# Kernel tuning notes

Measured on AMD Instinct MI355X. Metric: run time of the kernel, lower is better.

The kernel has to match this reference:

```python
import jax, jax.numpy as jnp
import numpy as np

N, E, D, H = 40000, 640000, 128, 8
DH = D // H  # out_feats per head
EPS = 1e-5


def _layernorm(x, g, b):
    mu = jnp.mean(x, axis=-1, keepdims=True)
    var = jnp.mean(jnp.square(x - mu), axis=-1, keepdims=True)
    return (x - mu) * jax.lax.rsqrt(var + EPS) * g + b


def setup_inputs() -> dict:
    key = jax.random.key(0)
    ks = jax.random.split(key, 12)
    s = 0.02
    return {
        "feat": jax.random.normal(ks[0], (N, D), dtype=jnp.float32),
        "src": jax.random.randint(ks[1], (E,), 0, N, dtype=jnp.int32),
        "dst": jax.random.randint(ks[2], (E,), 0, N, dtype=jnp.int32),
        "Wq": jax.random.normal(ks[3], (D, D), dtype=jnp.float32) * s,
        "Wk": jax.random.normal(ks[4], (D, D), dtype=jnp.float32) * s,
        "Wv": jax.random.normal(ks[5], (D, D), dtype=jnp.float32) * s,
        "ln1_g": jnp.ones((D,), jnp.float32),
        "ln1_b": jnp.zeros((D,), jnp.float32),
        "ln2_g": jnp.ones((D,), jnp.float32),
        "ln2_b": jnp.zeros((D,), jnp.float32),
        "W1": jax.random.normal(ks[6], (D, 4 * D), dtype=jnp.float32) * s,
        "b1": jnp.zeros((4 * D,), jnp.float32),
        "prelu_w": jnp.full((4 * D,), 0.25, jnp.float32),
        "W2": jax.random.normal(ks[7], (4 * D, D), dtype=jnp.float32) * s,
        "b2": jnp.zeros((D,), jnp.float32),
    }


def reference(feat, src, dst, Wq, Wk, Wv, ln1_g, ln1_b, ln2_g, ln2_b,
              W1, b1, prelu_w, W2, b2):
    n = feat.shape[0]
    feat_c = jax.lax.stop_gradient(feat)  # .clone().detach()
    q = (feat @ Wq).reshape(n, H, DH)
    k = (feat_c @ Wk).reshape(n, H, DH)
    v = (feat_c @ Wv).reshape(n, H, DH)

    # u_dot_v: per-edge, per-head dot product of k at src and q at dst
    scores = jnp.einsum('ehd,ehd->eh', k[src], q[dst]) / np.float32(np.sqrt(DH * H))

    # edge_softmax: softmax over incoming edges of each destination node
    smax = jax.ops.segment_max(scores, dst, num_segments=n)  # [N,H]
    sexp = jnp.exp(scores - smax[dst])
    ssum = jax.ops.segment_sum(sexp, dst, num_segments=n)
    a = sexp / ssum[dst]  # [E,H]  (attn_drop is eval no-op)

    # u_mul_e + sum: weighted scatter-aggregate of v[src] into dst
    msgs = v[src] * a[:, :, None]  # [E,H,DH]
    ft2 = jax.ops.segment_sum(msgs, dst, num_segments=n).reshape(n, D)

    rst = _layernorm(ft2 + feat, ln1_g, ln1_b)
    h = rst @ W1 + b1
    h = jnp.where(h >= 0, h, prelu_w * h)  # PReLU, per-channel
    ffn = h @ W2 + b2  # ffn_drop is eval no-op
    return _layernorm(rst + ffn, ln2_g, ln2_b)
```

## Files before the change

### kernel.cpp

```cpp
#include <hip/hip_runtime.h>
#include <hip/hip_bf16.h>
#include <math.h>

#define DIM 128
#define NHEAD 8
#define DHEAD 16
#define HID 512
#define LN_EPS 1e-5f
#define QSCALE 0.12751879104863297f

typedef __bf16 bf16x8 __attribute__((ext_vector_type(8)));
typedef float f32x4 __attribute__((ext_vector_type(4)));
typedef _Float16 f16x2 __attribute__((ext_vector_type(2)));

__device__ inline float bf2f(unsigned int bits16) {
    return __uint_as_float(bits16 << 16);
}
__device__ inline unsigned short f2bf(float f) {
    unsigned int u = __float_as_uint(f);
    unsigned int r = u + 0x7fff + ((u >> 16) & 1);
    return (unsigned short)(r >> 16);
}
__device__ inline unsigned short f2h(float f) {
    _Float16 h = (_Float16)f;
    return __builtin_bit_cast(unsigned short, h);
}
__device__ inline float edot2(unsigned int kw, f16x2 q) {
#if __has_builtin(__builtin_amdgcn_fdot2)
    return __builtin_amdgcn_fdot2(__builtin_bit_cast(f16x2, kw), q, 0.f, false);
#else
    f16x2 k = __builtin_bit_cast(f16x2, kw);
    return (float)k.x * (float)q.x + (float)k.y * (float)q.y;
#endif
}
__device__ inline float fexp2(float x) {
#if __has_builtin(__builtin_amdgcn_exp2f)
    return __builtin_amdgcn_exp2f(x);
#else
    return exp2f(x);
#endif
}

__device__ inline void gload_lds16(const void* g, void* l) {
    __builtin_amdgcn_global_load_lds(
        (const __attribute__((address_space(1))) unsigned int*)g,
        (__attribute__((address_space(3))) unsigned int*)l, 16, 0, 0);
}

__global__ __launch_bounds__(256) void prep_kernel(
        int* counts, int Nn,
        const float* __restrict__ feat, unsigned short* __restrict__ featb,
        const float* __restrict__ Wq, const float* __restrict__ Wk, const float* __restrict__ Wv,
        unsigned short* __restrict__ Wqkvt,
        const float* __restrict__ W1, unsigned short* __restrict__ W1t,
        const float* __restrict__ W2, unsigned short* __restrict__ W2t,
        int zb, int fb) {
    int blk = blockIdx.x, t = threadIdx.x;
    if (blk < zb) {
        int i = blk * 1024 + t * 4;
        if (i < Nn) *(int4*)(counts + i) = make_int4(0, 0, 0, 0);
    } else if (blk < fb) {
        int i = (blk - zb) * 256 + t;
        if (i < Nn * 32) {
            float4 v = *(const float4*)(feat + (size_t)i * 4);
            ushort4 o;
            o.x = f2bf(v.x); o.y = f2bf(v.y); o.z = f2bf(v.z); o.w = f2bf(v.w);
            *(ushort4*)(featb + (size_t)i * 4) = o;
        }
    } else {
        int b2_ = blk - fb;
        if (b2_ < 192) {
            int sec = b2_ >> 6;
            const float* W = sec == 0 ? Wq : (sec == 1 ? Wk : Wv);
            int o = (b2_ & 63) * 256 + t;
            int oc = o >> 7, orow = o & 127;
            Wqkvt[sec * 16384 + o] = f2bf(W[(size_t)orow * 128 + oc]);
        } else if (b2_ < 448) {
            int o = (b2_ - 192) * 256 + t;
            int oc = o >> 7, orow = o & 127;
            W1t[o] = f2bf(W1[(size_t)orow * 512 + oc]);
        } else {
            int o = (b2_ - 448) * 256 + t;
            int oc = o >> 9, orow = o & 511;
            W2t[o] = f2bf(W2[(size_t)orow * 128 + oc]);
        }
    }
}


__global__ void count_kernel(const int* __restrict__ dst, int* counts, int E) {
    int e = blockIdx.x * blockDim.x + threadIdx.x;
    if (e < E) atomicAdd(&counts[dst[e]], 1);
}

__global__ __launch_bounds__(256) void scanA_kernel(const int* __restrict__ counts, int* bsum, int Nn) {
    int blk = blockIdx.x, t = threadIdx.x;
    int i = blk * 1024 + t * 4;
    int s = 0;
    if (i < Nn) { int4 x = *(const int4*)(counts + i); s = x.x + x.y + x.z + x.w; }
#pragma unroll
    for (int off = 1; off < 64; off <<= 1) s += __shfl_xor(s, off, 64);
    __shared__ int wt[4];
    if ((t & 63) == 0) wt[t >> 6] = s;
    __syncthreads();
    if (t == 0) bsum[blk] = wt[0] + wt[1] + wt[2] + wt[3];
}

__global__ __launch_bounds__(256) void scanC_kernel(int* counts, const int* __restrict__ bsum,
                                                    int* offsets, int Nn, int NCH) {
    int blk = blockIdx.x, t = threadIdx.x, lane = t & 63, wv = t >> 6;
    __shared__ int wt[4];
    __shared__ int base_s;
    if (wv == 0) {
        int v = (lane < NCH) ? bsum[lane] : 0;
        int s = v;
#pragma unroll
        for (int off = 1; off < 64; off <<= 1) {
            int u = __shfl_up(s, off, 64);
            if (lane >= off) s += u;
        }
        int basev = (blk > 0) ? __shfl(s, blk - 1, 64) : 0;
        int tot = __shfl(s, NCH - 1, 64);
        if (lane == 0) {
            base_s = basev;
            if (blk == 0) offsets[Nn] = tot;
        }
    }
    int i = blk * 1024 + t * 4;
    int4 x = make_int4(0, 0, 0, 0);
    if (i < Nn) x = *(const int4*)(counts + i);
    int ts = x.x + x.y + x.z + x.w;
    int s = ts;
#pragma unroll
    for (int off = 1; off < 64; off <<= 1) {
        int u = __shfl_up(s, off, 64);
        if (lane >= off) s += u;
    }
    if (lane == 63) wt[wv] = s;
    __syncthreads();
    int woff = 0;
    for (int wi = 0; wi < wv; ++wi) woff += wt[wi];
    int excl = base_s + woff + (s - ts);
    if (i < Nn) {
        int o0 = excl, o1 = o0 + x.x, o2 = o1 + x.y, o3 = o2 + x.z;
        *(int4*)(offsets + i) = make_int4(o0, o1, o2, o3);
        *(int4*)(counts + i) = make_int4(o0, o1, o2, o3);
    }
}

__global__ void fill_kernel(const int* __restrict__ dst, const int* __restrict__ src,
                            int* cursor, int* srcs, int E) {
    int e = blockIdx.x * blockDim.x + threadIdx.x;
    if (e < E) {
        int pos = atomicAdd(&cursor[dst[e]], 1);
        srcs[pos] = src[e];
    }
}

#define QST 136
__global__ __launch_bounds__(256) void qkv_gemm(
        const unsigned short* __restrict__ A, const unsigned short* __restrict__ Bt,
        unsigned short* __restrict__ qb, unsigned short* __restrict__ kb,
        unsigned short* __restrict__ vb) {
    __shared__ unsigned short smem[128 * QST];
    unsigned short* As = smem;
    unsigned short* Bs = smem + 4096;
    int t = threadIdx.x;
    int wave = t >> 6, lane = t & 63;
    int wr = wave >> 1, wc = wave & 1;
    int lrow = lane & 15, kq = lane >> 4;
    int m0 = blockIdx.y * 128;
    int region = blockIdx.x;
    int n0 = region * 128;
    int srow = t >> 2, scol8 = (t & 3) * 8;

    f32x4 acc[4][4] = {};
    for (int k0 = 0; k0 < 128; k0 += 32) {
        gload_lds16(A + (size_t)(m0 + srow) * 128 + k0 + scol8,      As + t * 8);
        gload_lds16(A + (size_t)(m0 + 64 + srow) * 128 + k0 + scol8, As + 2048 + t * 8);
        gload_lds16(Bt + (size_t)(n0 + srow) * 128 + k0 + scol8,      Bs + t * 8);
        gload_lds16(Bt + (size_t)(n0 + 64 + srow) * 128 + k0 + scol8, Bs + 2048 + t * 8);
        __syncthreads();
        bf16x8 af[4], bfr[4];
#pragma unroll
        for (int mi = 0; mi < 4; ++mi)
            af[mi] = *(const bf16x8*)(&As[(wr * 64 + mi * 16 + lrow) * 32 + kq * 8]);
#pragma unroll
        for (int ni = 0; ni < 4; ++ni)
            bfr[ni] = *(const bf16x8*)(&Bs[(wc * 64 + ni * 16 + lrow) * 32 + kq * 8]);
#pragma unroll
        for (int mi = 0; mi < 4; ++mi)
#pragma unroll
            for (int ni = 0; ni < 4; ++ni)
                acc[mi][ni] = __builtin_amdgcn_mfma_f32_16x16x32_bf16(af[mi], bfr[ni], acc[mi][ni], 0, 0, 0);
        __syncthreads();
    }

    float scale = (region == 0) ? QSCALE : 1.f;
#pragma unroll
    for (int ni = 0; ni < 4; ++ni) {
        int col = wc * 64 + ni * 16 + lrow;
#pragma unroll
        for (int mi = 0; mi < 4; ++mi) {
#pragma unroll
            for (int r = 0; r < 4; ++r) {
                int row = wr * 64 + mi * 16 + kq * 4 + r;
                smem[row * QST + col] = f2h(acc[mi][ni][r] * scale);
            }
        }
    }
    __syncthreads();
    unsigned short* outp = (region == 0 ? qb : (region == 1 ? kb : vb)) + (size_t)m0 * 128;
#pragma unroll
    for (int i = 0; i < 8; ++i) {
        int chunk = i * 256 + t;
        int row = chunk >> 4, c16 = chunk & 15;
        *(float4*)(outp + (size_t)chunk * 8) = *(const float4*)(smem + row * QST + c16 * 8);
    }
}

__global__ __launch_bounds__(256) void agg_ln1_kernel(
        const unsigned short* __restrict__ qb, const unsigned short* __restrict__ kb,
        const unsigned short* __restrict__ vb,
        const float* __restrict__ feat,
        const int* __restrict__ srcs, const int* __restrict__ offsets,
        const float* __restrict__ g, const float* __restrict__ b,
        unsigned short* __restrict__ rstb, int n) {
    int node = blockIdx.x * 4 + (threadIdx.x >> 6);
    int lane = threadIdx.x & 63;
    if (node >= n) return;

    const unsigned int* q32 = (const unsigned int*)qb;
    const unsigned int* k32 = (const unsigned int*)kb;
    const unsigned int* v32 = (const unsigned int*)vb;
    f16x2 qp = __builtin_bit_cast(f16x2, q32[(size_t)node * 64 + lane]);

    int beg = offsets[node], end = offsets[node + 1];
    float m = -INFINITY, l = 0.f, a0 = 0.f, a1 = 0.f;

    int idx = beg;
    for (; idx + 8 <= end; idx += 8) {
        int s[8];
#pragma unroll
        for (int i = 0; i < 8; ++i) s[i] = srcs[idx + i];
        unsigned int kw[8], vw[8];
#pragma unroll
        for (int i = 0; i < 8; ++i) kw[i] = k32[(size_t)s[i] * 64 + lane];
#pragma unroll
        for (int i = 0; i < 8; ++i) vw[i] = v32[(size_t)s[i] * 64 + lane];
        float sc[8];
#pragma unroll
        for (int i = 0; i < 8; ++i) {
            float p = edot2(kw[i], qp);
            p += __shfl_xor(p, 1, 8);
            p += __shfl_xor(p, 2, 8);
            p += __shfl_xor(p, 4, 8);
            sc[i] = p;
        }
        float mn = m;
#pragma unroll
        for (int i = 0; i < 8; ++i) mn = fmaxf(mn, sc[i]);
        float f = fexp2(m - mn);
        float wsum = 0.f, d0 = 0.f, d1 = 0.f;
#pragma unroll
        for (int i = 0; i < 8; ++i) {
            float w = fexp2(sc[i] - mn);
            f16x2 vp = __builtin_bit_cast(f16x2, vw[i]);
            wsum += w;
            d0 = fmaf((float)vp.x, w, d0);
            d1 = fmaf((float)vp.y, w, d1);
        }
        l = l * f + wsum;
        a0 = a0 * f + d0;
        a1 = a1 * f + d1;
        m = mn;
    }
    for (; idx < end; ++idx) {
        int s = srcs[idx];
        unsigned int kw = k32[(size_t)s * 64 + lane];
        unsigned int vw = v32[(size_t)s * 64 + lane];
        float p = edot2(kw, qp);
        p += __shfl_xor(p, 1, 8);
        p += __shfl_xor(p, 2, 8);
        p += __shfl_xor(p, 4, 8);
        float mn = fmaxf(m, p);
        float f = fexp2(m - mn), w = fexp2(p - mn);
        f16x2 vp = __builtin_bit_cast(f16x2, vw);
        l = l * f + w;
        a0 = a0 * f + w * (float)vp.x;
        a1 = a1 * f + w * (float)vp.y;
        m = mn;
    }

    float inv = (l > 0.f) ? 1.f / l : 0.f;
    float2 fv = *(const float2*)(feat + (size_t)node * DIM + 2 * lane);
    float x0 = a0 * inv + fv.x;
    float x1 = a1 * inv + fv.y;

    float s1 = x0 + x1;
    float s2 = x0 * x0 + x1 * x1;
#pragma unroll
    for (int off = 1; off < 64; off <<= 1) {
        s1 += __shfl_xor(s1, off, 64);
        s2 += __shfl_xor(s2, off, 64);
    }
    float mean = s1 * (1.f / DIM);
    float var = s2 * (1.f / DIM) - mean * mean;
    float rinv = rsqrtf(var + LN_EPS);
    float g0 = g[2 * lane], g1 = g[2 * lane + 1];
    float b0 = b[2 * lane], b1 = b[2 * lane + 1];
    float o0 = (x0 - mean) * rinv * g0 + b0;
    float o1 = (x1 - mean) * rinv * g1 + b1;
    unsigned int packed = (unsigned int)f2bf(o0) | ((unsigned int)f2bf(o1) << 16);
    ((unsigned int*)rstb)[(size_t)node * 64 + lane] = packed;
}

#define FST 136
__global__ __launch_bounds__(256, 2) void ffn_fused_kernel(
        const unsigned short* __restrict__ rstb,
        const unsigned short* __restrict__ W1t, const float* __restrict__ b1,
        const float* __restrict__ prelu,
        const unsigned short* __restrict__ W2t, const float* __restrict__ b2,
        const float* __restrict__ g, const float* __restrict__ bb,
        float* __restrict__ out, int Nn) {
    __shared__ unsigned short As[128 * FST];
    __shared__ unsigned short Hs[128 * FST];
    __shared__ unsigned short Bs[128 * 32];
    __shared__ float red[128][4];

    int t = threadIdx.x, wave = t >> 6, lane = t & 63;
    int lrow = lane & 15, kq = lane >> 4;
    int wr = wave >> 1, wc = wave & 1;
    int m0 = blockIdx.x * 128;
    int srow = t >> 2, scol8 = (t & 3) * 8;

    {
        int row = t >> 1, half = t & 1;
        const float4* src = (const float4*)(rstb + (size_t)(m0 + row) * 128 + half * 64);
        float4* dst = (float4*)(As + row * FST + half * 64);
#pragma unroll
        for (int i = 0; i < 8; ++i) dst[i] = src[i];
    }
    f32x4 facc[4][4] = {};
    __syncthreads();

    for (int c = 0; c < 4; ++c) {
        f32x4 hacc[4][4] = {};
        for (int k0 = 0; k0 < 128; k0 += 32) {
            gload_lds16(W1t + (size_t)(c * 128 + srow) * 128 + k0 + scol8,      Bs + t * 8);
            gload_lds16(W1t + (size_t)(c * 128 + 64 + srow) * 128 + k0 + scol8, Bs + 2048 + t * 8);
            __syncthreads();
            bf16x8 hf[4], nf[4];
#pragma unroll
            for (int hi = 0; hi < 4; ++hi)
                hf[hi] = *(const bf16x8*)(&Bs[(wr * 64 + hi * 16 + lrow) * 32 + kq * 8]);
#pragma unroll
            for (int nj = 0; nj < 4; ++nj)
                nf[nj] = *(const bf16x8*)(&As[(wc * 64 + nj * 16 + lrow) * FST + k0 + kq * 8]);
#pragma unroll
            for (int hi = 0; hi < 4; ++hi)
#pragma unroll
                for (int nj = 0; nj < 4; ++nj)
                    hacc[hi][nj] = __builtin_amdgcn_mfma_f32_16x16x32_bf16(hf[hi], nf[nj], hacc[hi][nj], 0, 0, 0);
            __syncthreads();
        }
#pragma unroll
        for (int hi = 0; hi < 4; ++hi) {
            int hloc = wr * 64 + hi * 16 + kq * 4;
#pragma unroll
            for (int r = 0; r < 4; ++r) {
                int hg = c * 128 + hloc + r;
                float biv = b1[hg], pwv = prelu[hg];
#pragma unroll
                for (int nj = 0; nj < 4; ++nj) {
                    int node = wc * 64 + nj * 16 + lrow;
                    float v = hacc[hi][nj][r] + biv;
                    v = v >= 0.f ? v : pwv * v;
                    Hs[node * FST + hloc + r] = f2bf(v);
                }
            }
        }
        __syncthreads();
        for (int k0 = 0; k0 < 128; k0 += 32) {
            gload_lds16(W2t + (size_t)srow * 512 + c * 128 + k0 + scol8,        Bs + t * 8);
            gload_lds16(W2t + (size_t)(64 + srow) * 512 + c * 128 + k0 + scol8, Bs + 2048 + t * 8);
            __syncthreads();
            bf16x8 af[4], bf2r[4];
#pragma unroll
            for (int mi = 0; mi < 4; ++mi)
                af[mi] = *(const bf16x8*)(&Hs[(wr * 64 + mi * 16 + lrow) * FST + k0 + kq * 8]);
#pragma unroll
            for (int ni = 0; ni < 4; ++ni)
                bf2r[ni] = *(const bf16x8*)(&Bs[(wc * 64 + ni * 16 + lrow) * 32 + kq * 8]);
#pragma unroll
            for (int mi = 0; mi < 4; ++mi)
#pragma unroll
                for (int ni = 0; ni < 4; ++ni)
                    facc[mi][ni] = __builtin_amdgcn_mfma_f32_16x16x32_bf16(af[mi], bf2r[ni], facc[mi][ni], 0, 0, 0);
            __syncthreads();
        }
    }

    float b2v[4], gv[4], bv[4];
    int cols[4];
#pragma unroll
    for (int ni = 0; ni < 4; ++ni) {
        cols[ni] = wc * 64 + ni * 16 + lrow;
        b2v[ni] = b2[cols[ni]]; gv[ni] = g[cols[ni]]; bv[ni] = bb[cols[ni]];
    }
#pragma unroll
    for (int mi = 0; mi < 4; ++mi) {
#pragma unroll
        for (int r = 0; r < 4; ++r) {
            int rloc = wr * 64 + mi * 16 + kq * 4 + r;
            int row = m0 + rloc;
            float ps = 0.f, pq = 0.f;
#pragma unroll
            for (int ni = 0; ni < 4; ++ni) {
                float rsv = bf2f(rstb[(size_t)row * 128 + cols[ni]]);
                float v = facc[mi][ni][r] + b2v[ni] + rsv;
                facc[mi][ni][r] = v;
                ps += v; pq += v * v;
            }
#pragma unroll
            for (int off = 1; off < 16; off <<= 1) {
                ps += __shfl_xor(ps, off, 16);
                pq += __shfl_xor(pq, off, 16);
            }
            if (lrow == 0) { red[rloc][wc * 2] = ps; red[rloc][wc * 2 + 1] = pq; }
        }
    }
    __syncthreads();
#pragma unroll
    for (int mi = 0; mi < 4; ++mi) {
#pragma unroll
        for (int r = 0; r < 4; ++r) {
            int rloc = wr * 64 + mi * 16 + kq * 4 + r;
            int row = m0 + rloc;
            float s1 = red[rloc][0] + red[rloc][2];
            float s2 = red[rloc][1] + red[rloc][3];
            float mean = s1 * (1.f / DIM);
            float var = s2 * (1.f / DIM) - mean * mean;
            float rs = rsqrtf(var + LN_EPS);
            if (row < Nn) {
#pragma unroll
                for (int ni = 0; ni < 4; ++ni)
                    out[(size_t)row * 128 + cols[ni]] =
                        (facc[mi][ni][r] - mean) * rs * gv[ni] + bv[ni];
            }
        }
    }
}


extern "C" void kernel_launch(void* const* d_in, const int* in_sizes, int n_in,
                              void* d_out, int out_size, void* d_ws, size_t ws_size,
                              hipStream_t stream) {
    const float* feat   = (const float*)d_in[0];
    const int*   src    = (const int*)d_in[1];
    const int*   dst    = (const int*)d_in[2];
    const float* Wq     = (const float*)d_in[3];
    const float* Wk     = (const float*)d_in[4];
    const float* Wv     = (const float*)d_in[5];
    const float* ln1_g  = (const float*)d_in[6];
    const float* ln1_b  = (const float*)d_in[7];
    const float* ln2_g  = (const float*)d_in[8];
    const float* ln2_b  = (const float*)d_in[9];
    const float* W1     = (const float*)d_in[10];
    const float* b1     = (const float*)d_in[11];
    const float* prelu  = (const float*)d_in[12];
    const float* W2     = (const float*)d_in[13];
    const float* b2     = (const float*)d_in[14];
    float* out = (float*)d_out;

    const int Nn = in_sizes[0] / DIM;
    const int E  = in_sizes[1];
    const int MP = (Nn + 127) & ~127;

    char* w = (char*)d_ws;
    unsigned short* qb   = (unsigned short*)w; w += (size_t)MP * DIM * 2;
    unsigned short* kb   = (unsigned short*)w; w += (size_t)MP * DIM * 2;
    unsigned short* vb   = (unsigned short*)w; w += (size_t)MP * DIM * 2;
    unsigned short* rstb = (unsigned short*)w; w += (size_t)MP * DIM * 2;
    unsigned short* featb= (unsigned short*)w; w += (size_t)MP * DIM * 2;
    unsigned short* Wqkvt= (unsigned short*)w; w += 3 * DIM * DIM * 2;
    unsigned short* W1t  = (unsigned short*)w; w += (size_t)HID * DIM * 2;
    unsigned short* W2t  = (unsigned short*)w; w += (size_t)DIM * HID * 2;
    int* counts  = (int*)w;  w += (size_t)Nn * 4;
    int* offsets = (int*)w;  w += (size_t)(Nn + 4) * 4;
    int* bsum    = (int*)w;  w += 64 * 4;
    int* srcs    = (int*)w;

    const int NCH = (Nn + 1023) / 1024;
    const int zb = NCH;
    const int fb = zb + Nn / 8;

    prep_kernel<<<fb + 192 + 256 + 256, 256, 0, stream>>>(
        counts, Nn, feat, featb, Wq, Wk, Wv, Wqkvt, W1, W1t, W2, W2t, zb, fb);

    count_kernel<<<(E + 255) / 256, 256, 0, stream>>>(dst, counts, E);
    scanA_kernel<<<NCH, 256, 0, stream>>>(counts, bsum, Nn);
    scanC_kernel<<<NCH, 256, 0, stream>>>(counts, bsum, offsets, Nn, NCH);
    fill_kernel<<<(E + 255) / 256, 256, 0, stream>>>(dst, src, counts, srcs, E);

    {
        dim3 grid(3, MP / 128);
        qkv_gemm<<<grid, 256, 0, stream>>>(featb, Wqkvt, qb, kb, vb);
    }

    agg_ln1_kernel<<<(Nn + 3) / 4, 256, 0, stream>>>(qb, kb, vb, feat, srcs, offsets,
                                                     ln1_g, ln1_b, rstb, Nn);

    ffn_fused_kernel<<<MP / 128, 256, 0, stream>>>(rstb, W1t, b1, prelu,
                                                   W2t, b2, ln2_g, ln2_b, out, Nn);
}
```

Before: 262.6 us.

## Pack K/V as interleaved FP8 and split fused FFN into two GEMM kernels

Result: slower. 280.6 us (+6.8%).

```diff
diff --git a/kernel.cpp b/kernel.cpp
--- a/kernel.cpp
+++ b/kernel.cpp
@@ -11,6 +11,7 @@
 
 typedef __bf16 bf16x8 __attribute__((ext_vector_type(8)));
 typedef float f32x4 __attribute__((ext_vector_type(4)));
+typedef float f32x2 __attribute__((ext_vector_type(2)));
 typedef _Float16 f16x2 __attribute__((ext_vector_type(2)));
 
 __device__ inline float bf2f(unsigned int bits16) {
@@ -25,21 +26,15 @@
     _Float16 h = (_Float16)f;
     return __builtin_bit_cast(unsigned short, h);
 }
-__device__ inline float edot2(unsigned int kw, f16x2 q) {
-#if __has_builtin(__builtin_amdgcn_fdot2)
-    return __builtin_amdgcn_fdot2(__builtin_bit_cast(f16x2, kw), q, 0.f, false);
-#else
-    f16x2 k = __builtin_bit_cast(f16x2, kw);
-    return (float)k.x * (float)q.x + (float)k.y * (float)q.y;
-#endif
-}
-__device__ inline float fexp2(float x) {
-#if __has_builtin(__builtin_amdgcn_exp2f)
-    return __builtin_amdgcn_exp2f(x);
-#else
-    return exp2f(x);
-#endif
-}
+__device__ inline unsigned short pk_fp8(float a, float b) {
+    int r = __builtin_amdgcn_cvt_pk_fp8_f32(a, b, 0, false);
+    return (unsigned short)(r & 0xffff);
+}
+template <bool HI>
+__device__ inline f32x2 unpk_fp8(unsigned int w) {
+    return __builtin_amdgcn_cvt_pk_f32_fp8((int)w, HI);
+}
+__device__ inline float fexp2(float x) { return __builtin_amdgcn_exp2f(x); }
 
 __device__ inline void gload_lds16(const void* g, void* l) {
     __builtin_amdgcn_global_load_lds(
@@ -160,8 +155,7 @@
 #define QST 136
 __global__ __launch_bounds__(256) void qkv_gemm(
         const unsigned short* __restrict__ A, const unsigned short* __restrict__ Bt,
-        unsigned short* __restrict__ qb, unsigned short* __restrict__ kb,
-        unsigned short* __restrict__ vb) {
+        unsigned short* __restrict__ qb, unsigned short* __restrict__ kvp) {
     __shared__ unsigned short smem[128 * QST];
     unsigned short* As = smem;
     unsigned short* Bs = smem + 4096;
@@ -210,18 +204,31 @@
         }
     }
     __syncthreads();
-    unsigned short* outp = (region == 0 ? qb : (region == 1 ? kb : vb)) + (size_t)m0 * 128;
-#pragma unroll
-    for (int i = 0; i < 8; ++i) {
-        int chunk = i * 256 + t;
-        int row = chunk >> 4, c16 = chunk & 15;
-        *(float4*)(outp + (size_t)chunk * 8) = *(const float4*)(smem + row * QST + c16 * 8);
+    if (region == 0) {
+        unsigned short* outp = qb + (size_t)m0 * 128;
+#pragma unroll
+        for (int i = 0; i < 8; ++i) {
+            int chunk = i * 256 + t;
+            int row = chunk >> 4, c16 = chunk & 15;
+            *(float4*)(outp + (size_t)chunk * 8) = *(const float4*)(smem + row * QST + c16 * 8);
+        }
+    } else {
+        int off = region - 1;
+        int row = t >> 1, half = t & 1;
+        unsigned short* dstp = kvp + (size_t)(m0 + row) * 128 + off;
+        const unsigned short* sp = smem + row * QST;
+#pragma unroll
+        for (int jj = 0; jj < 32; ++jj) {
+            int j = half * 32 + jj;
+            float f0 = (float)__builtin_bit_cast(_Float16, sp[2 * j]);
+            float f1 = (float)__builtin_bit_cast(_Float16, sp[2 * j + 1]);
+            dstp[2 * j] = pk_fp8(f0, f1);
+        }
     }
 }
 
 __global__ __launch_bounds__(256) void agg_ln1_kernel(
-        const unsigned short* __restrict__ qb, const unsigned short* __restrict__ kb,
-        const unsigned short* __restrict__ vb,
+        const unsigned short* __restrict__ qb, const unsigned short* __restrict__ kvp,
         const float* __restrict__ feat,
         const int* __restrict__ srcs, const int* __restrict__ offsets,
         const float* __restrict__ g, const float* __restrict__ b,
@@ -230,10 +237,10 @@
     int lane = threadIdx.x & 63;
     if (node >= n) return;
 
-    const unsigned int* q32 = (const unsigned int*)qb;
-    const unsigned int* k32 = (const unsigned int*)kb;
-    const unsigned int* v32 = (const unsigned int*)vb;
-    f16x2 qp = __builtin_bit_cast(f16x2, q32[(size_t)node * 64 + lane]);
+    unsigned int qw = ((const unsigned int*)qb)[(size_t)node * 64 + lane];
+    f16x2 qp = __builtin_bit_cast(f16x2, qw);
+    float q0 = (float)qp.x, q1 = (float)qp.y;
+    const unsigned int* kv32 = (const unsigned int*)kvp;
 
     int beg = offsets[node], end = offsets[node + 1];
     float m = -INFINITY, l = 0.f, a0 = 0.f, a1 = 0.f;
@@ -243,15 +250,14 @@
         int s[8];
 #pragma unroll
         for (int i = 0; i < 8; ++i) s[i] = srcs[idx + i];
-        unsigned int kw[8], vw[8];
-#pragma unroll
-        for (int i = 0; i < 8; ++i) kw[i] = k32[(size_t)s[i] * 64 + lane];
-#pragma unroll
-        for (int i = 0; i < 8; ++i) vw[i] = v32[(size_t)s[i] * 64 + lane];
+        unsigned int w[8];
+#pragma unroll
+        for (int i = 0; i < 8; ++i) w[i] = kv32[(size_t)s[i] * 64 + lane];
         float sc[8];
 #pragma unroll
         for (int i = 0; i < 8; ++i) {
-            float p = edot2(kw[i], qp);
+            f32x2 kk = unpk_fp8<false>(w[i]);
+            float p = fmaf(kk.x, q0, kk.y * q1);
             p += __shfl_xor(p, 1, 8);
             p += __shfl_xor(p, 2, 8);
             p += __shfl_xor(p, 4, 8);
@@ -264,11 +270,11 @@
         float wsum = 0.f, d0 = 0.f, d1 = 0.f;
 #pragma unroll
         for (int i = 0; i < 8; ++i) {
-            float w = fexp2(sc[i] - mn);
-            f16x2 vp = __builtin_bit_cast(f16x2, vw[i]);
-            wsum += w;
-            d0 = fmaf((float)vp.x, w, d0);
-            d1 = fmaf((float)vp.y, w, d1);
+            float ww = fexp2(sc[i] - mn);
+            f32x2 vv = unpk_fp8<true>(w[i]);
+            wsum += ww;
+            d0 = fmaf(vv.x, ww, d0);
+            d1 = fmaf(vv.y, ww, d1);
         }
         l = l * f + wsum;
         a0 = a0 * f + d0;
@@ -277,18 +283,18 @@
     }
     for (; idx < end; ++idx) {
         int s = srcs[idx];
-        unsigned int kw = k32[(size_t)s * 64 + lane];
-        unsigned int vw = v32[(size_t)s * 64 + lane];
-        float p = edot2(kw, qp);
+        unsigned int w = kv32[(size_t)s * 64 + lane];
+        f32x2 kk = unpk_fp8<false>(w);
+        float p = fmaf(kk.x, q0, kk.y * q1);
         p += __shfl_xor(p, 1, 8);
         p += __shfl_xor(p, 2, 8);
         p += __shfl_xor(p, 4, 8);
         float mn = fmaxf(m, p);
-        float f = fexp2(m - mn), w = fexp2(p - mn);
-        f16x2 vp = __builtin_bit_cast(f16x2, vw);
-        l = l * f + w;
-        a0 = a0 * f + w * (float)vp.x;
-        a1 = a1 * f + w * (float)vp.y;
+        float f = fexp2(m - mn), ww = fexp2(p - mn);
+        f32x2 vv = unpk_fp8<true>(w);
+        l = l * f + ww;
+        a0 = a0 * f + ww * vv.x;
+        a1 = a1 * f + ww * vv.y;
         m = mn;
     }
 
@@ -315,90 +321,104 @@
     ((unsigned int*)rstb)[(size_t)node * 64 + lane] = packed;
 }
 
-#define FST 136
-__global__ __launch_bounds__(256, 2) void ffn_fused_kernel(
+__global__ __launch_bounds__(256) void ffn1_gemm(
+        const unsigned short* __restrict__ A, const unsigned short* __restrict__ Bt,
+        unsigned short* __restrict__ hid,
+        const float* __restrict__ b1, const float* __restrict__ prelu) {
+    __shared__ unsigned short smem[128 * QST];
+    unsigned short* As = smem;
+    unsigned short* Bs = smem + 4096;
+    int t = threadIdx.x;
+    int wave = t >> 6, lane = t & 63;
+    int wr = wave >> 1, wc = wave & 1;
+    int lrow = lane & 15, kq = lane >> 4;
+    int m0 = blockIdx.y * 128;
+    int n0 = blockIdx.x * 128;
+    int srow = t >> 2, scol8 = (t & 3) * 8;
+
+    f32x4 acc[4][4] = {};
+    for (int k0 = 0; k0 < 128; k0 += 32) {
+        gload_lds16(A + (size_t)(m0 + srow) * 128 + k0 + scol8,      As + t * 8);
+        gload_lds16(A + (size_t)(m0 + 64 + srow) * 128 + k0 + scol8, As + 2048 + t * 8);
+        gload_lds16(Bt + (size_t)(n0 + srow) * 128 + k0 + scol8,      Bs + t * 8);
+        gload_lds16(Bt + (size_t)(n0 + 64 + srow) * 128 + k0 + scol8, Bs + 2048 + t * 8);
+        __syncthreads();
+        bf16x8 af[4], bfr[4];
+#pragma unroll
+        for (int mi = 0; mi < 4; ++mi)
+            af[mi] = *(const bf16x8*)(&As[(wr * 64 + mi * 16 + lrow) * 32 + kq * 8]);
+#pragma unroll
+        for (int ni = 0; ni < 4; ++ni)
+            bfr[ni] = *(const bf16x8*)(&Bs[(wc * 64 + ni * 16 + lrow) * 32 + kq * 8]);
+#pragma unroll
+        for (int mi = 0; mi < 4; ++mi)
+#pragma unroll
+            for (int ni = 0; ni < 4; ++ni)
+                acc[mi][ni] = __builtin_amdgcn_mfma_f32_16x16x32_bf16(af[mi], bfr[ni], acc[mi][ni], 0, 0, 0);
+        __syncthreads();
+    }
+
+#pragma unroll
+    for (int ni = 0; ni < 4; ++ni) {
+        int col = wc * 64 + ni * 16 + lrow;
+        int cg = n0 + col;
+        float biv = b1[cg], pwv = prelu[cg];
+#pragma unroll
+        for (int mi = 0; mi < 4; ++mi) {
+#pragma unroll
+            for (int r = 0; r < 4; ++r) {
+                int row = wr * 64 + mi * 16 + kq * 4 + r;
+                float v = acc[mi][ni][r] + biv;
+                v = v >= 0.f ? v : pwv * v;
+                smem[row * QST + col] = f2bf(v);
+            }
+        }
+    }
+    __syncthreads();
+#pragma unroll
+    for (int i = 0; i < 8; ++i) {
+        int chunk = i * 256 + t;
+        int row = chunk >> 4, c16 = chunk & 15;
+        *(float4*)(hid + (size_t)(m0 + row) * 512 + n0 + c16 * 8) =
+            *(const float4*)(smem + row * QST + c16 * 8);
+    }
+}
+
+__global__ __launch_bounds__(256) void ffn2_ln2_kernel(
+        const unsigned short* __restrict__ hid, const unsigned short* __restrict__ W2t,
         const unsigned short* __restrict__ rstb,
-        const unsigned short* __restrict__ W1t, const float* __restrict__ b1,
-        const float* __restrict__ prelu,
-        const unsigned short* __restrict__ W2t, const float* __restrict__ b2,
-        const float* __restrict__ g, const float* __restrict__ bb,
+        const float* __restrict__ b2, const float* __restrict__ g, const float* __restrict__ bb,
         float* __restrict__ out, int Nn) {
-    __shared__ unsigned short As[128 * FST];
-    __shared__ unsigned short Hs[128 * FST];
+    __shared__ unsigned short As[128 * 32];
     __shared__ unsigned short Bs[128 * 32];
     __shared__ float red[128][4];
-
-    int t = threadIdx.x, wave = t >> 6, lane = t & 63;
+    int t = threadIdx.x;
+    int wave = t >> 6, lane = t & 63;
+    int wr = wave >> 1, wc = wave & 1;
     int lrow = lane & 15, kq = lane >> 4;
-    int wr = wave >> 1, wc = wave & 1;
     int m0 = blockIdx.x * 128;
     int srow = t >> 2, scol8 = (t & 3) * 8;
 
-    {
-        int row = t >> 1, half = t & 1;
-        const float4* src = (const float4*)(rstb + (size_t)(m0 + row) * 128 + half * 64);
-        float4* dst = (float4*)(As + row * FST + half * 64);
-#pragma unroll
-        for (int i = 0; i < 8; ++i) dst[i] = src[i];
-    }
-    f32x4 facc[4][4] = {};
-    __syncthreads();
-
-    for (int c = 0; c < 4; ++c) {
-        f32x4 hacc[4][4] = {};
-        for (int k0 = 0; k0 < 128; k0 += 32) {
-            gload_lds16(W1t + (size_t)(c * 128 + srow) * 128 + k0 + scol8,      Bs + t * 8);
-            gload_lds16(W1t + (size_t)(c * 128 + 64 + srow) * 128 + k0 + scol8, Bs + 2048 + t * 8);
-            __syncthreads();
-            bf16x8 hf[4], nf[4];
-#pragma unroll
-            for (int hi = 0; hi < 4; ++hi)
-                hf[hi] = *(const bf16x8*)(&Bs[(wr * 64 + hi * 16 + lrow) * 32 + kq * 8]);
-#pragma unroll
-            for (int nj = 0; nj < 4; ++nj)
-                nf[nj] = *(const bf16x8*)(&As[(wc * 64 + nj * 16 + lrow) * FST + k0 + kq * 8]);
-#pragma unroll
-            for (int hi = 0; hi < 4; ++hi)
-#pragma unroll
-                for (int nj = 0; nj < 4; ++nj)
-                    hacc[hi][nj] = __builtin_amdgcn_mfma_f32_16x16x32_bf16(hf[hi], nf[nj], hacc[hi][nj], 0, 0, 0);
-            __syncthreads();
-        }
-#pragma unroll
-        for (int hi = 0; hi < 4; ++hi) {
-            int hloc = wr * 64 + hi * 16 + kq * 4;
-#pragma unroll
-            for (int r = 0; r < 4; ++r) {
-                int hg = c * 128 + hloc + r;
-                float biv = b1[hg], pwv = prelu[hg];
-#pragma unroll
-                for (int nj = 0; nj < 4; ++nj) {
-                    int node = wc * 64 + nj * 16 + lrow;
-                    float v = hacc[hi][nj][r] + biv;
-                    v = v >= 0.f ? v : pwv * v;
-                    Hs[node * FST + hloc + r] = f2bf(v);
-                }
-            }
-        }
+    f32x4 acc[4][4] = {};
+    for (int k0 = 0; k0 < 512; k0 += 32) {
+        gload_lds16(hid + (size_t)(m0 + srow) * 512 + k0 + scol8,      As + t * 8);
+        gload_lds16(hid + (size_t)(m0 + 64 + srow) * 512 + k0 + scol8, As + 2048 + t * 8);
+        gload_lds16(W2t + (size_t)srow * 512 + k0 + scol8,             Bs + t * 8);
+        gload_lds16(W2t + (size_t)(64 + srow) * 512 + k0 + scol8,      Bs + 2048 + t * 8);
         __syncthreads();
-        for (int k0 = 0; k0 < 128; k0 += 32) {
-            gload_lds16(W2t + (size_t)srow * 512 + c * 128 + k0 + scol8,        Bs + t * 8);
-            gload_lds16(W2t + (size_t)(64 + srow) * 512 + c * 128 + k0 + scol8, Bs + 2048 + t * 8);
-            __syncthreads();
-            bf16x8 af[4], bf2r[4];
-#pragma unroll
-            for (int mi = 0; mi < 4; ++mi)
-                af[mi] = *(const bf16x8*)(&Hs[(wr * 64 + mi * 16 + lrow) * FST + k0 + kq * 8]);
+        bf16x8 af[4], bfr[4];
+#pragma unroll
+        for (int mi = 0; mi < 4; ++mi)
+            af[mi] = *(const bf16x8*)(&As[(wr * 64 + mi * 16 + lrow) * 32 + kq * 8]);
+#pragma unroll
+        for (int ni = 0; ni < 4; ++ni)
+            bfr[ni] = *(const bf16x8*)(&Bs[(wc * 64 + ni * 16 + lrow) * 32 + kq * 8]);
+#pragma unroll
+        for (int mi = 0; mi < 4; ++mi)
 #pragma unroll
             for (int ni = 0; ni < 4; ++ni)
-                bf2r[ni] = *(const bf16x8*)(&Bs[(wc * 64 + ni * 16 + lrow) * 32 + kq * 8]);
-#pragma unroll
-            for (int mi = 0; mi < 4; ++mi)
-#pragma unroll
-                for (int ni = 0; ni < 4; ++ni)
-                    facc[mi][ni] = __builtin_amdgcn_mfma_f32_16x16x32_bf16(af[mi], bf2r[ni], facc[mi][ni], 0, 0, 0);
-            __syncthreads();
-        }
+                acc[mi][ni] = __builtin_amdgcn_mfma_f32_16x16x32_bf16(af[mi], bfr[ni], acc[mi][ni], 0, 0, 0);
+        __syncthreads();
     }
 
     float b2v[4], gv[4], bv[4];
@@ -418,8 +438,8 @@
 #pragma unroll
             for (int ni = 0; ni < 4; ++ni) {
                 float rsv = bf2f(rstb[(size_t)row * 128 + cols[ni]]);
-                float v = facc[mi][ni][r] + b2v[ni] + rsv;
-                facc[mi][ni][r] = v;
+                float v = acc[mi][ni][r] + b2v[ni] + rsv;
+                acc[mi][ni][r] = v;
                 ps += v; pq += v * v;
             }
 #pragma unroll
@@ -446,7 +466,7 @@
 #pragma unroll
                 for (int ni = 0; ni < 4; ++ni)
                     out[(size_t)row * 128 + cols[ni]] =
-                        (facc[mi][ni][r] - mean) * rs * gv[ni] + bv[ni];
+                        (acc[mi][ni][r] - mean) * rs * gv[ni] + bv[ni];
             }
         }
     }
@@ -479,10 +499,10 @@
 
     char* w = (char*)d_ws;
     unsigned short* qb   = (unsigned short*)w; w += (size_t)MP * DIM * 2;
-    unsigned short* kb   = (unsigned short*)w; w += (size_t)MP * DIM * 2;
-    unsigned short* vb   = (unsigned short*)w; w += (size_t)MP * DIM * 2;
+    unsigned short* kvp  = (unsigned short*)w; w += (size_t)MP * DIM * 2;
     unsigned short* rstb = (unsigned short*)w; w += (size_t)MP * DIM * 2;
     unsigned short* featb= (unsigned short*)w; w += (size_t)MP * DIM * 2;
+    unsigned short* hid  = (unsigned short*)w; w += (size_t)MP * HID * 2;
     unsigned short* Wqkvt= (unsigned short*)w; w += 3 * DIM * DIM * 2;
     unsigned short* W1t  = (unsigned short*)w; w += (size_t)HID * DIM * 2;
     unsigned short* W2t  = (unsigned short*)w; w += (size_t)DIM * HID * 2;
@@ -505,12 +525,16 @@
 
     {
         dim3 grid(3, MP / 128);
-        qkv_gemm<<<grid, 256, 0, stream>>>(featb, Wqkvt, qb, kb, vb);
-    }
-
-    agg_ln1_kernel<<<(Nn + 3) / 4, 256, 0, stream>>>(qb, kb, vb, feat, srcs, offsets,
+        qkv_gemm<<<grid, 256, 0, stream>>>(featb, Wqkvt, qb, kvp);
+    }
+
+    agg_ln1_kernel<<<(Nn + 3) / 4, 256, 0, stream>>>(qb, kvp, feat, srcs, offsets,
                                                      ln1_g, ln1_b, rstb, Nn);
 
-    ffn_fused_kernel<<<MP / 128, 256, 0, stream>>>(rstb, W1t, b1, prelu,
-                                                   W2t, b2, ln2_g, ln2_b, out, Nn);
-}
+    {
+        dim3 grid(4, MP / 128);
+        ffn1_gemm<<<grid, 256, 0, stream>>>(rstb, W1t, hid, b1, prelu);
+    }
+
+    ffn2_ln2_kernel<<<MP / 128, 256, 0, stream>>>(hid, W2t, rstb, b2, ln2_g, ln2_b, out, Nn);
+}
```
